# Kernel tuning notes

Measured on AMD Instinct MI355X. Metric: run time of the kernel, lower is better.

## Reference

```python
import jax, jax.numpy as jnp
import numpy as np


def setup_inputs() -> dict:
    key = jax.random.key(0)
    ks = jax.random.split(key, 7)
    B, T, C, H = 8, 2048, 2048, 128
    x = jax.random.normal(ks[0], (B, T, C), dtype=jnp.float32)
    Wq = jax.random.normal(ks[1], (C, H), dtype=jnp.float32) * (C ** -0.5)
    bq = jax.random.normal(ks[2], (H,), dtype=jnp.float32) * 0.02
    Wk = jax.random.normal(ks[3], (C, H), dtype=jnp.float32) * (C ** -0.5)
    bk = jax.random.normal(ks[4], (H,), dtype=jnp.float32) * 0.02
    Wv = jax.random.normal(ks[5], (C, H), dtype=jnp.float32) * (C ** -0.5)
    bv = jax.random.normal(ks[6], (H,), dtype=jnp.float32) * 0.02
    return {"x": x, "Wq": Wq, "bq": bq, "Wk": Wk, "bk": bk, "Wv": Wv, "bv": bv}


def reference(x, Wq, bq, Wk, bk, Wv, bv):
    # Single-head causal self-attention (dropout in eval mode = identity).
    B, T, C = x.shape
    H = Wq.shape[1]
    Q = jnp.einsum("btc,ch->bth", x, Wq) + bq  # [B,T,H]
    K = jnp.einsum("btc,ch->bth", x, Wk) + bk
    V = jnp.einsum("btc,ch->bth", x, Wv) + bv
    scale = H ** -0.5
    wei = jnp.einsum("bth,bsh->bts", Q, K) * scale  # [B,T,T]
    causal = jnp.tril(jnp.ones((T, T), dtype=bool))
    wei = jnp.where(causal, wei, -jnp.inf)
    wei = jax.nn.softmax(wei, axis=-1)
    out = jnp.einsum("bts,bsh->bth", wei, V)  # [B,T,H]
    return out
```

## Files before the change

kernel.cpp:

```cpp
#include <hip/hip_runtime.h>

typedef float f32x4 __attribute__((ext_vector_type(4)));
typedef short short8 __attribute__((ext_vector_type(8)));
typedef unsigned short ushort8 __attribute__((ext_vector_type(8)));

#define WS_Q  786432
#define WS_K  2883584
#define WS_VT 4980736

__device__ __forceinline__ unsigned short f2bf(float x) {
    unsigned u = __float_as_uint(x);
    u += 0x7FFFu + ((u >> 16) & 1u);
    return (unsigned short)(u >> 16);
}

__device__ __forceinline__ int swz128(int row, int cbyte) {
    return row * 128 + (cbyte ^ ((row & 7) << 4));
}

__global__ __launch_bounds__(256) void wt_kernel(const float* __restrict__ Wq,
        const float* __restrict__ Wk, const float* __restrict__ Wv,
        unsigned short* __restrict__ ws) {
    __shared__ __align__(16) unsigned short tile[64][136];
    int mat = blockIdx.x >> 5, ct = blockIdx.x & 31;
    const float* W = (mat == 0) ? Wq : ((mat == 1) ? Wk : Wv);
    int cbase = ct * 64;
    int tid = threadIdx.x;
#pragma unroll
    for (int p = 0; p < 8; p++) {
        int fidx = p * 256 + tid;
        int row = fidx >> 5;
        int c4 = (fidx & 31) << 2;
        float4 v = *(const float4*)&W[(size_t)(cbase + row) * 128 + c4];
        tile[row][c4 + 0] = f2bf(v.x);
        tile[row][c4 + 1] = f2bf(v.y);
        tile[row][c4 + 2] = f2bf(v.z);
        tile[row][c4 + 3] = f2bf(v.w);
    }
    __syncthreads();
    int h = tid >> 1, seg = tid & 1;
    unsigned short* dst = ws + mat * 262144 + (ct * 2 + seg) * 4096 + h * 32;
#pragma unroll
    for (int q4 = 0; q4 < 4; q4++) {
        ushort8 pk;
#pragma unroll
        for (int e = 0; e < 8; e++) pk[e] = tile[seg * 32 + q4 * 8 + e][h];
        *(ushort8*)(dst + q4 * 8) = pk;
    }
}

__global__ __launch_bounds__(256, 3) void qkv_kernel(const float* __restrict__ x,
        const float* __restrict__ bq, const float* __restrict__ bk,
        const float* __restrict__ bv, unsigned short* __restrict__ ws) {
    __shared__ __align__(16) unsigned short lds[4][6144];
    int bid = blockIdx.x;
    int g = bid / 24, j = bid - g * 24;
    int which = j >> 3;
    int mt = g * 8 + (j & 7);
    const unsigned short* WTt = ws + which * 262144;
    const float* x0 = x + (size_t)mt * 64 * 2048;
    int tid = threadIdx.x, lane = tid & 63, wid = tid >> 6;
    int lr = lane & 15, lg = lane >> 4;
    int m0 = (wid >> 1) * 32, n0 = (wid & 1) * 64;

    const float* bias = (which == 0) ? bq : ((which == 1) ? bk : bv);
    float bb[4];
#pragma unroll
    for (int j2 = 0; j2 < 4; j2++) bb[j2] = bias[n0 + j2 * 16 + lr];
    asm volatile("" : "+v"(bb[0]), "+v"(bb[1]), "+v"(bb[2]), "+v"(bb[3]));
    asm volatile("s_waitcnt vmcnt(0)" ::: "memory");

    int rowA = tid >> 2, ca = tid & 3;
    const float* aSrc = x0 + (size_t)rowA * 2048 + ca * 8;
    int aDst = rowA * 64 + ((ca ^ ((rowA >> 1) & 3)) << 4);

    int bsrc0, bsrc1, bdst0, bdst1;
    {
        int idx0 = (0 * 4 + wid) * 64 + lane;
        int h0 = idx0 >> 2, c0 = idx0 & 3;
        bsrc0 = h0 * 32 + ((c0 ^ ((h0 >> 1) & 3)) << 3);
        bdst0 = (0 * 4 + wid) * 1024;
        int idx1 = (1 * 4 + wid) * 64 + lane;
        int h1 = idx1 >> 2, c1 = idx1 & 3;
        bsrc1 = h1 * 32 + ((c1 ^ ((h1 >> 1) & 3)) << 3);
        bdst1 = (1 * 4 + wid) * 1024;
    }

    int aOff0, aOff1, bOff0, bOff1, bOff2, bOff3;
    {
        int r0 = m0 + 0 * 16 + lr; aOff0 = r0 * 64 + ((lg ^ ((r0 >> 1) & 3)) << 4);
        int r1 = m0 + 1 * 16 + lr; aOff1 = r1 * 64 + ((lg ^ ((r1 >> 1) & 3)) << 4);
        int s0 = n0 + 0 * 16 + lr; bOff0 = s0 * 64 + ((lg ^ ((s0 >> 1) & 3)) << 4);
        int s1 = n0 + 1 * 16 + lr; bOff1 = s1 * 64 + ((lg ^ ((s1 >> 1) & 3)) << 4);
        int s2 = n0 + 2 * 16 + lr; bOff2 = s2 * 64 + ((lg ^ ((s2 >> 1) & 3)) << 4);
        int s3 = n0 + 3 * 16 + lr; bOff3 = s3 * 64 + ((lg ^ ((s3 >> 1) & 3)) << 4);
    }

    f32x4 acc[2][4];
#pragma unroll
    for (int i = 0; i < 2; i++)
#pragma unroll
        for (int j3 = 0; j3 < 4; j3++) acc[i][j3] = (f32x4){0.f, 0.f, 0.f, 0.f};
    float4 rA[4][2];

#define ISSUE_A(SLOT, T) do { \
        const float* ap_ = aSrc + (size_t)(T) * 32; \
        rA[SLOT][0] = *(const float4*)ap_; \
        rA[SLOT][1] = *(const float4*)(ap_ + 4); \
    } while (0)
#define ISSUE_B(BUF, T) do { \
        const unsigned short* bs_ = WTt + (size_t)(T) * 4096; \
        char* bd_ = (char*)&lds[BUF][2048]; \
        __builtin_amdgcn_global_load_lds((const __attribute__((address_space(1))) unsigned*)(bs_ + bsrc0), \
            (__attribute__((address_space(3))) unsigned*)(bd_ + bdst0), 16, 0, 0); \
        __builtin_amdgcn_global_load_lds((const __attribute__((address_space(1))) unsigned*)(bs_ + bsrc1), \
            (__attribute__((address_space(3))) unsigned*)(bd_ + bdst1), 16, 0, 0); \
    } while (0)
#define WRITE_A(SLOT, BUF) do { \
        const float* f_ = (const float*)&rA[SLOT][0]; \
        ushort8 pk_; \
        pk_[0] = f2bf(f_[0]); pk_[1] = f2bf(f_[1]); pk_[2] = f2bf(f_[2]); pk_[3] = f2bf(f_[3]); \
        pk_[4] = f2bf(f_[4]); pk_[5] = f2bf(f_[5]); pk_[6] = f2bf(f_[6]); pk_[7] = f2bf(f_[7]); \
        *(ushort8*)((char*)&lds[BUF][0] + aDst) = pk_; \
    } while (0)

#define QKV_BODY(U, T, STAGE, WAIT4, WAIT0, WRITE, BAR) do { \
        const char* Ab_ = (const char*)&lds[U][0]; \
        const char* Bb_ = (const char*)&lds[U][2048]; \
        short8 av0 = *(const short8*)(Ab_ + aOff0); \
        short8 av1 = *(const short8*)(Ab_ + aOff1); \
        short8 bv0 = *(const short8*)(Bb_ + bOff0); \
        short8 bv1 = *(const short8*)(Bb_ + bOff1); \
        short8 bv2 = *(const short8*)(Bb_ + bOff2); \
        short8 bv3 = *(const short8*)(Bb_ + bOff3); \
        if (STAGE) { ISSUE_A(((T) + 3) & 3, (T) + 3); ISSUE_B(((U) + 3) & 3, (T) + 3); } \
        acc[0][0] = __builtin_amdgcn_mfma_f32_16x16x32_bf16(av0, bv0, acc[0][0], 0, 0, 0); \
        acc[0][1] = __builtin_amdgcn_mfma_f32_16x16x32_bf16(av0, bv1, acc[0][1], 0, 0, 0); \
        acc[0][2] = __builtin_amdgcn_mfma_f32_16x16x32_bf16(av0, bv2, acc[0][2], 0, 0, 0); \
        acc[0][3] = __builtin_amdgcn_mfma_f32_16x16x32_bf16(av0, bv3, acc[0][3], 0, 0, 0); \
        acc[1][0] = __builtin_amdgcn_mfma_f32_16x16x32_bf16(av1, bv0, acc[1][0], 0, 0, 0); \
        acc[1][1] = __builtin_amdgcn_mfma_f32_16x16x32_bf16(av1, bv1, acc[1][1], 0, 0, 0); \
        acc[1][2] = __builtin_amdgcn_mfma_f32_16x16x32_bf16(av1, bv2, acc[1][2], 0, 0, 0); \
        acc[1][3] = __builtin_amdgcn_mfma_f32_16x16x32_bf16(av1, bv3, acc[1][3], 0, 0, 0); \
        if (STAGE)      { asm volatile("s_waitcnt vmcnt(8)" ::: "memory"); } \
        else if (WAIT4) { asm volatile("s_waitcnt vmcnt(4)" ::: "memory"); } \
        else if (WAIT0) { asm volatile("s_waitcnt vmcnt(0)" ::: "memory"); } \
        if (WRITE) { \
            WRITE_A(((T) + 1) & 3, ((U) + 1) & 3); \
            asm volatile("s_waitcnt lgkmcnt(0)" ::: "memory"); \
        } \
        if (BAR) __builtin_amdgcn_s_barrier(); \
    } while (0)

    ISSUE_A(0, 0); ISSUE_B(0, 0);
    ISSUE_A(1, 1); ISSUE_B(1, 1);
    ISSUE_A(2, 2); ISSUE_B(2, 2);
    asm volatile("s_waitcnt vmcnt(8)" ::: "memory");
    WRITE_A(0, 0);
    asm volatile("s_waitcnt lgkmcnt(0)" ::: "memory");
    __builtin_amdgcn_s_barrier();

    for (int to = 0; to < 15; to++) {
        int T0 = to * 4;
        QKV_BODY(0, T0 + 0, true, false, false, true, true);
        QKV_BODY(1, T0 + 1, true, false, false, true, true);
        QKV_BODY(2, T0 + 2, true, false, false, true, true);
        QKV_BODY(3, T0 + 3, true, false, false, true, true);
    }
    QKV_BODY(0, 60, true,  false, false, true,  true);
    QKV_BODY(1, 61, false, true,  false, true,  true);
    QKV_BODY(2, 62, false, false, true,  true,  true);
    QKV_BODY(3, 63, false, false, false, false, false);

    if (which < 2) {
        unsigned short* outp = ws + ((which == 0) ? WS_Q : WS_K);
        float sc = (which == 0) ? 0.08838834764831845f : 1.0f;
#pragma unroll
        for (int i = 0; i < 2; i++)
#pragma unroll
            for (int j3 = 0; j3 < 4; j3++) {
                int h = n0 + j3 * 16 + lr;
#pragma unroll
                for (int r = 0; r < 4; r++) {
                    int t = mt * 64 + m0 + i * 16 + (lg << 2) + r;
                    outp[(size_t)t * 128 + h] = f2bf((acc[i][j3][r] + bb[j3]) * sc);
                }
            }
    } else {
        __syncthreads();
        unsigned short* sm = &lds[0][0];
#pragma unroll
        for (int i = 0; i < 2; i++)
#pragma unroll
            for (int j3 = 0; j3 < 4; j3++) {
                int h = n0 + j3 * 16 + lr;
#pragma unroll
                for (int r = 0; r < 4; r++) {
                    int tl = m0 + i * 16 + (lg << 2) + r;
                    sm[tl * 136 + h] = f2bf(acc[i][j3][r] + bb[j3]);
                }
            }
        __syncthreads();
        int h = tid & 127, seg = tid >> 7;
        int b2 = mt >> 5;
        int tin = (mt & 31) * 64 + seg * 32;
        unsigned short* vt = ws + WS_VT + ((size_t)b2 * 128 + h) * 2048 + tin;
#pragma unroll
        for (int q4 = 0; q4 < 4; q4++) {
            ushort8 pk;
#pragma unroll
            for (int e = 0; e < 8; e++) pk[e] = sm[(seg * 32 + q4 * 8 + e) * 136 + h];
            *(ushort8*)(vt + q4 * 8) = pk;
        }
    }
#undef QKV_BODY
#undef WRITE_A
#undef ISSUE_B
#undef ISSUE_A
}

__global__ __launch_bounds__(256, 2) void attn_kernel(const unsigned short* __restrict__ ws,
        float* __restrict__ out) {
    __shared__ __align__(16) float o_lds[4][32][128];
    __shared__ float ml[4][2][32];
    int b = blockIdx.x;
    int qi = 63 - (int)blockIdx.y;
    int qbase = qi * 32;
    int tid = threadIdx.x, lane = tid & 63, w = tid >> 6;
    int lr = lane & 15, lg = lane >> 4;
    const unsigned short* Qb = ws + WS_Q + (size_t)b * 2048 * 128;
    const unsigned short* Kb = ws + WS_K + (size_t)b * 2048 * 128;
    const unsigned short* Vt = ws + WS_VT + (size_t)b * 128 * 2048;
    char* p_lds = (char*)&o_lds[w][0][0];

    short8 qf[2][4];
#pragma unroll
    for (int i = 0; i < 2; i++)
#pragma unroll
        for (int kf = 0; kf < 4; kf++)
            qf[i][kf] = *(const short8*)&Qb[(size_t)(qbase + i * 16 + lr) * 128 + kf * 32 + lg * 8];

    f32x4 o[2][8];
#pragma unroll
    for (int i = 0; i < 2; i++)
#pragma unroll
        for (int jn = 0; jn < 8; jn++) o[i][jn] = (f32x4){0.f, 0.f, 0.f, 0.f};
    float mrow[2][4], lrow[2][4];
#pragma unroll
    for (int i = 0; i < 2; i++)
#pragma unroll
        for (int r = 0; r < 4; r++) { mrow[i][r] = -__builtin_inff(); lrow[i][r] = 0.f; }

    int ntiles = qi / 2 + 1;
    for (int ti = w; ti < ntiles; ti += 4) {
        int sb = ti * 64;
        f32x4 s[2][4];
#pragma unroll
        for (int i = 0; i < 2; i++)
#pragma unroll
            for (int nf = 0; nf < 4; nf++) s[i][nf] = (f32x4){0.f, 0.f, 0.f, 0.f};
        {
            short8 kb[4][4];
#pragma unroll
            for (int nf = 0; nf < 4; nf++)
#pragma unroll
                for (int kf = 0; kf < 4; kf++)
                    kb[nf][kf] = *(const short8*)&Kb[(size_t)(sb + nf * 16 + lr) * 128 + kf * 32 + lg * 8];
#pragma unroll
            for (int kf = 0; kf < 4; kf++)
#pragma unroll
                for (int i = 0; i < 2; i++)
#pragma unroll
                    for (int nf = 0; nf < 4; nf++)
                        s[i][nf] = __builtin_amdgcn_mfma_f32_16x16x32_bf16(qf[i][kf], kb[nf][kf], s[i][nf], 0, 0, 0);
        }
        if (sb + 63 > qbase) {
#pragma unroll
            for (int i = 0; i < 2; i++)
#pragma unroll
                for (int nf = 0; nf < 4; nf++)
#pragma unroll
                    for (int r = 0; r < 4; r++) {
                        int sg = sb + nf * 16 + lr;
                        int qg = qbase + i * 16 + (lg << 2) + r;
                        if (sg > qg) s[i][nf][r] = -__builtin_inff();
                    }
        }
        float alpha[2][4];
#pragma unroll
        for (int i = 0; i < 2; i++)
#pragma unroll
            for (int r = 0; r < 4; r++) {
                float pm = fmaxf(fmaxf(s[i][0][r], s[i][1][r]), fmaxf(s[i][2][r], s[i][3][r]));
                pm = fmaxf(pm, __shfl_xor(pm, 1));
                pm = fmaxf(pm, __shfl_xor(pm, 2));
                pm = fmaxf(pm, __shfl_xor(pm, 4));
                pm = fmaxf(pm, __shfl_xor(pm, 8));
                float mn = fmaxf(mrow[i][r], pm);
                alpha[i][r] = __expf(mrow[i][r] - mn);
                mrow[i][r] = mn;
            }
#pragma unroll
        for (int i = 0; i < 2; i++)
#pragma unroll
            for (int r = 0; r < 4; r++) {
                float rs = 0.f;
#pragma unroll
                for (int nf = 0; nf < 4; nf++) {
                    float p = __expf(s[i][nf][r] - mrow[i][r]);
                    s[i][nf][r] = p;
                    rs += p;
                }
                rs += __shfl_xor(rs, 1);
                rs += __shfl_xor(rs, 2);
                rs += __shfl_xor(rs, 4);
                rs += __shfl_xor(rs, 8);
                lrow[i][r] = lrow[i][r] * alpha[i][r] + rs;
            }
#pragma unroll
        for (int i = 0; i < 2; i++)
#pragma unroll
            for (int jn = 0; jn < 8; jn++)
#pragma unroll
                for (int r = 0; r < 4; r++) o[i][jn][r] *= alpha[i][r];
#pragma unroll
        for (int i = 0; i < 2; i++)
#pragma unroll
            for (int nf = 0; nf < 4; nf++)
#pragma unroll
                for (int r = 0; r < 4; r++) {
                    int row = i * 16 + (lg << 2) + r;
                    int cb2 = (nf * 16 + lr) * 2;
                    *(unsigned short*)(p_lds + swz128(row, cb2)) = f2bf(s[i][nf][r]);
                }
        asm volatile("s_waitcnt lgkmcnt(0)" ::: "memory");
        short8 pa[2][2];
#pragma unroll
        for (int i = 0; i < 2; i++)
#pragma unroll
            for (int kf = 0; kf < 2; kf++)
                pa[i][kf] = *(const short8*)(p_lds + swz128(i * 16 + lr, kf * 64 + lg * 16));
        short8 vb[8][2];
#pragma unroll
        for (int nf = 0; nf < 8; nf++)
#pragma unroll
            for (int kf = 0; kf < 2; kf++)
                vb[nf][kf] = *(const short8*)&Vt[(size_t)(nf * 16 + lr) * 2048 + sb + kf * 32 + lg * 8];
#pragma unroll
        for (int i = 0; i < 2; i++)
#pragma unroll
            for (int nf = 0; nf < 8; nf++)
#pragma unroll
                for (int kf = 0; kf < 2; kf++)
                    o[i][nf] = __builtin_amdgcn_mfma_f32_16x16x32_bf16(pa[i][kf], vb[nf][kf], o[i][nf], 0, 0, 0);
    }
#pragma unroll
    for (int i = 0; i < 2; i++)
#pragma unroll
        for (int r = 0; r < 4; r++) {
            int q = i * 16 + (lg << 2) + r;
            ml[w][0][q] = mrow[i][r];
            ml[w][1][q] = lrow[i][r];
        }
    asm volatile("s_waitcnt lgkmcnt(0)" ::: "memory");
#pragma unroll
    for (int i = 0; i < 2; i++)
#pragma unroll
        for (int jn = 0; jn < 8; jn++)
#pragma unroll
            for (int r = 0; r < 4; r++)
                o_lds[w][i * 16 + (lg << 2) + r][jn * 16 + lr] = o[i][jn][r];
    __syncthreads();
    int q = tid >> 3, h0 = (tid & 7) << 4;
    float mg = fmaxf(fmaxf(ml[0][0][q], ml[1][0][q]), fmaxf(ml[2][0][q], ml[3][0][q]));
    float scw[4], den = 0.f;
#pragma unroll
    for (int w4 = 0; w4 < 4; w4++) {
        scw[w4] = __expf(ml[w4][0][q] - mg);
        den += scw[w4] * ml[w4][1][q];
    }
    float inv = 1.0f / den;
    float* op = out + ((size_t)b * 2048 + qbase + q) * 128 + h0;
#pragma unroll
    for (int jj = 0; jj < 4; jj++) {
        f32x4 a4 = (f32x4){0.f, 0.f, 0.f, 0.f};
#pragma unroll
        for (int w4 = 0; w4 < 4; w4++) {
            f32x4 v = *(const f32x4*)&o_lds[w4][q][h0 + jj * 4];
            a4 += scw[w4] * v;
        }
        a4 *= inv;
        *(f32x4*)(op + jj * 4) = a4;
    }
}

extern "C" void kernel_launch(void* const* d_in, const int* in_sizes, int n_in,
                              void* d_out, int out_size, void* d_ws, size_t ws_size,
                              hipStream_t stream) {
    (void)in_sizes; (void)n_in; (void)out_size; (void)ws_size;
    const float* x  = (const float*)d_in[0];
    const float* Wq = (const float*)d_in[1];
    const float* bq = (const float*)d_in[2];
    const float* Wk = (const float*)d_in[3];
    const float* bk = (const float*)d_in[4];
    const float* Wv = (const float*)d_in[5];
    const float* bv = (const float*)d_in[6];
    unsigned short* ws = (unsigned short*)d_ws;
    float* out = (float*)d_out;

    wt_kernel<<<96, 256, 0, stream>>>(Wq, Wk, Wv, ws);
    qkv_kernel<<<768, 256, 0, stream>>>(x, bq, bk, bv, ws);
    attn_kernel<<<dim3(8, 64), 256, 0, stream>>>(ws, out);
}
```

Baseline: 106.9 us.

## Enlarge QKV projection tile to 128 rows with triple-buffered LDS pipeline

Result: slower. 246.5 us (+130.6%).

```diff
diff --git a/kernel.cpp b/kernel.cpp
--- a/kernel.cpp
+++ b/kernel.cpp
@@ -12,6 +12,15 @@
     unsigned u = __float_as_uint(x);
     u += 0x7FFFu + ((u >> 16) & 1u);
     return (unsigned short)(u >> 16);
+}
+
+__device__ __forceinline__ short8 cvt8(float4 lo, float4 hi) {
+    union { unsigned u[4]; short8 s; } r;
+    asm("v_cvt_pk_bf16_f32 %0, %1, %2" : "=v"(r.u[0]) : "v"(lo.x), "v"(lo.y));
+    asm("v_cvt_pk_bf16_f32 %0, %1, %2" : "=v"(r.u[1]) : "v"(lo.z), "v"(lo.w));
+    asm("v_cvt_pk_bf16_f32 %0, %1, %2" : "=v"(r.u[2]) : "v"(hi.x), "v"(hi.y));
+    asm("v_cvt_pk_bf16_f32 %0, %1, %2" : "=v"(r.u[3]) : "v"(hi.z), "v"(hi.w));
+    return r.s;
 }
 
 __device__ __forceinline__ int swz128(int row, int cbyte) {
@@ -52,88 +61,90 @@
 __global__ __launch_bounds__(256, 3) void qkv_kernel(const float* __restrict__ x,
         const float* __restrict__ bq, const float* __restrict__ bk,
         const float* __restrict__ bv, unsigned short* __restrict__ ws) {
-    __shared__ __align__(16) unsigned short lds[4][6144];
+    __shared__ __align__(16) char lds_raw[3][16384];
     int bid = blockIdx.x;
-    int g = bid / 24, j = bid - g * 24;
-    int which = j >> 3;
-    int mt = g * 8 + (j & 7);
-    const unsigned short* WTt = ws + which * 262144;
-    const float* x0 = x + (size_t)mt * 64 * 2048;
+    int matrix = bid >> 7;
+    int strip = bid & 127;
+    const unsigned short* WTt = ws + matrix * 262144;
+    const float* x0 = x + (size_t)strip * 128 * 2048;
     int tid = threadIdx.x, lane = tid & 63, wid = tid >> 6;
     int lr = lane & 15, lg = lane >> 4;
-    int m0 = (wid >> 1) * 32, n0 = (wid & 1) * 64;
-
-    const float* bias = (which == 0) ? bq : ((which == 1) ? bk : bv);
+    int m0 = (wid >> 1) * 64, n0 = (wid & 1) * 64;
+
+    const float* bias = (matrix == 0) ? bq : ((matrix == 1) ? bk : bv);
     float bb[4];
 #pragma unroll
     for (int j2 = 0; j2 < 4; j2++) bb[j2] = bias[n0 + j2 * 16 + lr];
     asm volatile("" : "+v"(bb[0]), "+v"(bb[1]), "+v"(bb[2]), "+v"(bb[3]));
     asm volatile("s_waitcnt vmcnt(0)" ::: "memory");
 
-    int rowA = tid >> 2, ca = tid & 3;
-    const float* aSrc = x0 + (size_t)rowA * 2048 + ca * 8;
-    int aDst = rowA * 64 + ((ca ^ ((rowA >> 1) & 3)) << 4);
+    int rowA = tid >> 1, hf = tid & 1;
+    const float* aSrc = x0 + (size_t)rowA * 2048 + hf * 16;
+    int aDst0 = rowA * 64 + (((hf * 2 + 0) ^ ((rowA >> 1) & 3)) << 4);
+    int aDst1 = rowA * 64 + (((hf * 2 + 1) ^ ((rowA >> 1) & 3)) << 4);
 
     int bsrc0, bsrc1, bdst0, bdst1;
     {
-        int idx0 = (0 * 4 + wid) * 64 + lane;
-        int h0 = idx0 >> 2, c0 = idx0 & 3;
-        bsrc0 = h0 * 32 + ((c0 ^ ((h0 >> 1) & 3)) << 3);
-        bdst0 = (0 * 4 + wid) * 1024;
-        int idx1 = (1 * 4 + wid) * 64 + lane;
-        int h1 = idx1 >> 2, c1 = idx1 & 3;
-        bsrc1 = h1 * 32 + ((c1 ^ ((h1 >> 1) & 3)) << 3);
-        bdst1 = (1 * 4 + wid) * 1024;
-    }
-
-    int aOff0, aOff1, bOff0, bOff1, bOff2, bOff3;
+        int sig0 = wid * 64 + lane;
+        int r0 = sig0 >> 2, s0 = (sig0 & 3) ^ ((r0 >> 1) & 3);
+        bsrc0 = r0 * 32 + s0 * 8;  bdst0 = wid * 1024;
+        int sig1 = (4 + wid) * 64 + lane;
+        int r1 = sig1 >> 2, s1 = (sig1 & 3) ^ ((r1 >> 1) & 3);
+        bsrc1 = r1 * 32 + s1 * 8;  bdst1 = (4 + wid) * 1024;
+    }
+
+    int aOff0, aOff1, aOff2, aOff3, bOff0, bOff1, bOff2, bOff3;
     {
         int r0 = m0 + 0 * 16 + lr; aOff0 = r0 * 64 + ((lg ^ ((r0 >> 1) & 3)) << 4);
         int r1 = m0 + 1 * 16 + lr; aOff1 = r1 * 64 + ((lg ^ ((r1 >> 1) & 3)) << 4);
-        int s0 = n0 + 0 * 16 + lr; bOff0 = s0 * 64 + ((lg ^ ((s0 >> 1) & 3)) << 4);
-        int s1 = n0 + 1 * 16 + lr; bOff1 = s1 * 64 + ((lg ^ ((s1 >> 1) & 3)) << 4);
-        int s2 = n0 + 2 * 16 + lr; bOff2 = s2 * 64 + ((lg ^ ((s2 >> 1) & 3)) << 4);
-        int s3 = n0 + 3 * 16 + lr; bOff3 = s3 * 64 + ((lg ^ ((s3 >> 1) & 3)) << 4);
-    }
-
-    f32x4 acc[2][4];
-#pragma unroll
-    for (int i = 0; i < 2; i++)
+        int r2 = m0 + 2 * 16 + lr; aOff2 = r2 * 64 + ((lg ^ ((r2 >> 1) & 3)) << 4);
+        int r3 = m0 + 3 * 16 + lr; aOff3 = r3 * 64 + ((lg ^ ((r3 >> 1) & 3)) << 4);
+        int h0 = n0 + 0 * 16 + lr; bOff0 = 8192 + h0 * 64 + ((lg ^ ((h0 >> 1) & 3)) << 4);
+        int h1 = n0 + 1 * 16 + lr; bOff1 = 8192 + h1 * 64 + ((lg ^ ((h1 >> 1) & 3)) << 4);
+        int h2 = n0 + 2 * 16 + lr; bOff2 = 8192 + h2 * 64 + ((lg ^ ((h2 >> 1) & 3)) << 4);
+        int h3 = n0 + 3 * 16 + lr; bOff3 = 8192 + h3 * 64 + ((lg ^ ((h3 >> 1) & 3)) << 4);
+    }
+
+    f32x4 acc[4][4];
+#pragma unroll
+    for (int i = 0; i < 4; i++)
 #pragma unroll
         for (int j3 = 0; j3 < 4; j3++) acc[i][j3] = (f32x4){0.f, 0.f, 0.f, 0.f};
-    float4 rA[4][2];
+    float4 rA[2][4];
 
 #define ISSUE_A(SLOT, T) do { \
         const float* ap_ = aSrc + (size_t)(T) * 32; \
         rA[SLOT][0] = *(const float4*)ap_; \
         rA[SLOT][1] = *(const float4*)(ap_ + 4); \
+        rA[SLOT][2] = *(const float4*)(ap_ + 8); \
+        rA[SLOT][3] = *(const float4*)(ap_ + 12); \
     } while (0)
 #define ISSUE_B(BUF, T) do { \
         const unsigned short* bs_ = WTt + (size_t)(T) * 4096; \
-        char* bd_ = (char*)&lds[BUF][2048]; \
+        char* bd_ = &lds_raw[BUF][8192]; \
         __builtin_amdgcn_global_load_lds((const __attribute__((address_space(1))) unsigned*)(bs_ + bsrc0), \
             (__attribute__((address_space(3))) unsigned*)(bd_ + bdst0), 16, 0, 0); \
         __builtin_amdgcn_global_load_lds((const __attribute__((address_space(1))) unsigned*)(bs_ + bsrc1), \
             (__attribute__((address_space(3))) unsigned*)(bd_ + bdst1), 16, 0, 0); \
     } while (0)
 #define WRITE_A(SLOT, BUF) do { \
-        const float* f_ = (const float*)&rA[SLOT][0]; \
-        ushort8 pk_; \
-        pk_[0] = f2bf(f_[0]); pk_[1] = f2bf(f_[1]); pk_[2] = f2bf(f_[2]); pk_[3] = f2bf(f_[3]); \
-        pk_[4] = f2bf(f_[4]); pk_[5] = f2bf(f_[5]); pk_[6] = f2bf(f_[6]); pk_[7] = f2bf(f_[7]); \
-        *(ushort8*)((char*)&lds[BUF][0] + aDst) = pk_; \
+        short8 p0_ = cvt8(rA[SLOT][0], rA[SLOT][1]); \
+        short8 p1_ = cvt8(rA[SLOT][2], rA[SLOT][3]); \
+        *(short8*)(&lds_raw[BUF][0] + aDst0) = p0_; \
+        *(short8*)(&lds_raw[BUF][0] + aDst1) = p1_; \
     } while (0)
 
-#define QKV_BODY(U, T, STAGE, WAIT4, WAIT0, WRITE, BAR) do { \
-        const char* Ab_ = (const char*)&lds[U][0]; \
-        const char* Bb_ = (const char*)&lds[U][2048]; \
-        short8 av0 = *(const short8*)(Ab_ + aOff0); \
-        short8 av1 = *(const short8*)(Ab_ + aOff1); \
-        short8 bv0 = *(const short8*)(Bb_ + bOff0); \
-        short8 bv1 = *(const short8*)(Bb_ + bOff1); \
-        short8 bv2 = *(const short8*)(Bb_ + bOff2); \
-        short8 bv3 = *(const short8*)(Bb_ + bOff3); \
-        if (STAGE) { ISSUE_A(((T) + 3) & 3, (T) + 3); ISSUE_B(((U) + 3) & 3, (T) + 3); } \
+#define QKV_BODY(U, T, STAGE, WAIT0, WRITE, BAR) do { \
+        const char* Lb_ = &lds_raw[U][0]; \
+        short8 av0 = *(const short8*)(Lb_ + aOff0); \
+        short8 av1 = *(const short8*)(Lb_ + aOff1); \
+        short8 av2 = *(const short8*)(Lb_ + aOff2); \
+        short8 av3 = *(const short8*)(Lb_ + aOff3); \
+        short8 bv0 = *(const short8*)(Lb_ + bOff0); \
+        short8 bv1 = *(const short8*)(Lb_ + bOff1); \
+        short8 bv2 = *(const short8*)(Lb_ + bOff2); \
+        short8 bv3 = *(const short8*)(Lb_ + bOff3); \
+        if (STAGE) { ISSUE_A((T) & 1, (T) + 2); ISSUE_B(((U) + 2) % 3, (T) + 2); } \
         acc[0][0] = __builtin_amdgcn_mfma_f32_16x16x32_bf16(av0, bv0, acc[0][0], 0, 0, 0); \
         acc[0][1] = __builtin_amdgcn_mfma_f32_16x16x32_bf16(av0, bv1, acc[0][1], 0, 0, 0); \
         acc[0][2] = __builtin_amdgcn_mfma_f32_16x16x32_bf16(av0, bv2, acc[0][2], 0, 0, 0); \
@@ -142,11 +153,18 @@
         acc[1][1] = __builtin_amdgcn_mfma_f32_16x16x32_bf16(av1, bv1, acc[1][1], 0, 0, 0); \
         acc[1][2] = __builtin_amdgcn_mfma_f32_16x16x32_bf16(av1, bv2, acc[1][2], 0, 0, 0); \
         acc[1][3] = __builtin_amdgcn_mfma_f32_16x16x32_bf16(av1, bv3, acc[1][3], 0, 0, 0); \
-        if (STAGE)      { asm volatile("s_waitcnt vmcnt(8)" ::: "memory"); } \
-        else if (WAIT4) { asm volatile("s_waitcnt vmcnt(4)" ::: "memory"); } \
+        acc[2][0] = __builtin_amdgcn_mfma_f32_16x16x32_bf16(av2, bv0, acc[2][0], 0, 0, 0); \
+        acc[2][1] = __builtin_amdgcn_mfma_f32_16x16x32_bf16(av2, bv1, acc[2][1], 0, 0, 0); \
+        acc[2][2] = __builtin_amdgcn_mfma_f32_16x16x32_bf16(av2, bv2, acc[2][2], 0, 0, 0); \
+        acc[2][3] = __builtin_amdgcn_mfma_f32_16x16x32_bf16(av2, bv3, acc[2][3], 0, 0, 0); \
+        acc[3][0] = __builtin_amdgcn_mfma_f32_16x16x32_bf16(av3, bv0, acc[3][0], 0, 0, 0); \
+        acc[3][1] = __builtin_amdgcn_mfma_f32_16x16x32_bf16(av3, bv1, acc[3][1], 0, 0, 0); \
+        acc[3][2] = __builtin_amdgcn_mfma_f32_16x16x32_bf16(av3, bv2, acc[3][2], 0, 0, 0); \
+        acc[3][3] = __builtin_amdgcn_mfma_f32_16x16x32_bf16(av3, bv3, acc[3][3], 0, 0, 0); \
+        if (STAGE)      { asm volatile("s_waitcnt vmcnt(6)" ::: "memory"); } \
         else if (WAIT0) { asm volatile("s_waitcnt vmcnt(0)" ::: "memory"); } \
         if (WRITE) { \
-            WRITE_A(((T) + 1) & 3, ((U) + 1) & 3); \
+            WRITE_A(((T) + 1) & 1, ((U) + 1) % 3); \
             asm volatile("s_waitcnt lgkmcnt(0)" ::: "memory"); \
         } \
         if (BAR) __builtin_amdgcn_s_barrier(); \
@@ -154,43 +172,41 @@
 
     ISSUE_A(0, 0); ISSUE_B(0, 0);
     ISSUE_A(1, 1); ISSUE_B(1, 1);
-    ISSUE_A(2, 2); ISSUE_B(2, 2);
-    asm volatile("s_waitcnt vmcnt(8)" ::: "memory");
+    asm volatile("s_waitcnt vmcnt(6)" ::: "memory");
     WRITE_A(0, 0);
     asm volatile("s_waitcnt lgkmcnt(0)" ::: "memory");
     __builtin_amdgcn_s_barrier();
 
-    for (int to = 0; to < 15; to++) {
-        int T0 = to * 4;
-        QKV_BODY(0, T0 + 0, true, false, false, true, true);
-        QKV_BODY(1, T0 + 1, true, false, false, true, true);
-        QKV_BODY(2, T0 + 2, true, false, false, true, true);
-        QKV_BODY(3, T0 + 3, true, false, false, true, true);
-    }
-    QKV_BODY(0, 60, true,  false, false, true,  true);
-    QKV_BODY(1, 61, false, true,  false, true,  true);
-    QKV_BODY(2, 62, false, false, true,  true,  true);
-    QKV_BODY(3, 63, false, false, false, false, false);
-
-    if (which < 2) {
-        unsigned short* outp = ws + ((which == 0) ? WS_Q : WS_K);
-        float sc = (which == 0) ? 0.08838834764831845f : 1.0f;
-#pragma unroll
-        for (int i = 0; i < 2; i++)
+    for (int to = 0; to < 20; to++) {
+        int T0 = to * 3;
+        QKV_BODY(0, T0 + 0, true, false, true, true);
+        QKV_BODY(1, T0 + 1, true, false, true, true);
+        QKV_BODY(2, T0 + 2, true, false, true, true);
+    }
+    QKV_BODY(0, 60, true,  false, true,  true);
+    QKV_BODY(1, 61, true,  false, true,  true);
+    QKV_BODY(2, 62, false, true,  true,  true);
+    QKV_BODY(0, 63, false, false, false, false);
+
+    if (matrix < 2) {
+        unsigned short* outp = ws + ((matrix == 0) ? WS_Q : WS_K);
+        float sc = (matrix == 0) ? 0.08838834764831845f : 1.0f;
+#pragma unroll
+        for (int i = 0; i < 4; i++)
 #pragma unroll
             for (int j3 = 0; j3 < 4; j3++) {
                 int h = n0 + j3 * 16 + lr;
 #pragma unroll
                 for (int r = 0; r < 4; r++) {
-                    int t = mt * 64 + m0 + i * 16 + (lg << 2) + r;
-                    outp[(size_t)t * 128 + h] = f2bf((acc[i][j3][r] + bb[j3]) * sc);
+                    size_t t = (size_t)strip * 128 + m0 + i * 16 + (lg << 2) + r;
+                    outp[t * 128 + h] = f2bf((acc[i][j3][r] + bb[j3]) * sc);
                 }
             }
     } else {
         __syncthreads();
-        unsigned short* sm = &lds[0][0];
-#pragma unroll
-        for (int i = 0; i < 2; i++)
+        unsigned short* sm = (unsigned short*)&lds_raw[0][0];
+#pragma unroll
+        for (int i = 0; i < 4; i++)
 #pragma unroll
             for (int j3 = 0; j3 < 4; j3++) {
                 int h = n0 + j3 * 16 + lr;
@@ -201,16 +217,16 @@
                 }
             }
         __syncthreads();
-        int h = tid & 127, seg = tid >> 7;
-        int b2 = mt >> 5;
-        int tin = (mt & 31) * 64 + seg * 32;
-        unsigned short* vt = ws + WS_VT + ((size_t)b2 * 128 + h) * 2048 + tin;
-#pragma unroll
-        for (int q4 = 0; q4 < 4; q4++) {
+        int h2 = tid >> 1, seg = tid & 1;
+        int batch = strip >> 4;
+        int tin = (strip & 15) * 128 + seg * 64;
+        unsigned short* vt = ws + WS_VT + ((size_t)batch * 128 + h2) * 2048 + tin;
+#pragma unroll
+        for (int q8 = 0; q8 < 8; q8++) {
             ushort8 pk;
 #pragma unroll
-            for (int e = 0; e < 8; e++) pk[e] = sm[(seg * 32 + q4 * 8 + e) * 136 + h];
-            *(ushort8*)(vt + q4 * 8) = pk;
+            for (int e = 0; e < 8; e++) pk[e] = sm[(seg * 64 + q8 * 8 + e) * 136 + h2];
+            *(ushort8*)(vt + q8 * 8) = pk;
         }
     }
 #undef QKV_BODY
@@ -409,6 +425,6 @@
     float* out = (float*)d_out;
 
     wt_kernel<<<96, 256, 0, stream>>>(Wq, Wk, Wv, ws);
-    qkv_kernel<<<768, 256, 0, stream>>>(x, bq, bk, bv, ws);
+    qkv_kernel<<<384, 256, 0, stream>>>(x, bq, bk, bv, ws);
     attn_kernel<<<dim3(8, 64), 256, 0, stream>>>(ws, out);
 }
```

## Restructure QKV projection to 64-wide K tiles with double buffering

Applied to the files above, without the earlier changes.

Measured after the change: 113.2 us. 1.06x slower.

```diff
diff --git a/kernel.cpp b/kernel.cpp
--- a/kernel.cpp
+++ b/kernel.cpp
@@ -3,6 +3,9 @@
 typedef float f32x4 __attribute__((ext_vector_type(4)));
 typedef short short8 __attribute__((ext_vector_type(8)));
 typedef unsigned short ushort8 __attribute__((ext_vector_type(8)));
+
+#define AS1 __attribute__((address_space(1)))
+#define AS3 __attribute__((address_space(3)))
 
 #define WS_Q  786432
 #define WS_K  2883584
@@ -12,6 +15,15 @@
     unsigned u = __float_as_uint(x);
     u += 0x7FFFu + ((u >> 16) & 1u);
     return (unsigned short)(u >> 16);
+}
+
+__device__ __forceinline__ short8 cvt8(float4 lo, float4 hi) {
+    union { unsigned u[4]; short8 s; } r;
+    asm("v_cvt_pk_bf16_f32 %0, %1, %2" : "=v"(r.u[0]) : "v"(lo.x), "v"(lo.y));
+    asm("v_cvt_pk_bf16_f32 %0, %1, %2" : "=v"(r.u[1]) : "v"(lo.z), "v"(lo.w));
+    asm("v_cvt_pk_bf16_f32 %0, %1, %2" : "=v"(r.u[2]) : "v"(hi.x), "v"(hi.y));
+    asm("v_cvt_pk_bf16_f32 %0, %1, %2" : "=v"(r.u[3]) : "v"(hi.z), "v"(hi.w));
+    return r.s;
 }
 
 __device__ __forceinline__ int swz128(int row, int cbyte) {
@@ -39,61 +51,53 @@
     }
     __syncthreads();
     int h = tid >> 1, seg = tid & 1;
-    unsigned short* dst = ws + mat * 262144 + (ct * 2 + seg) * 4096 + h * 32;
+    unsigned short* base = ws + mat * 262144 + ct * 8192 + h * 64;
 #pragma unroll
     for (int q4 = 0; q4 < 4; q4++) {
         ushort8 pk;
 #pragma unroll
         for (int e = 0; e < 8; e++) pk[e] = tile[seg * 32 + q4 * 8 + e][h];
-        *(ushort8*)(dst + q4 * 8) = pk;
+        int g = seg * 4 + q4;
+        *(ushort8*)(base + ((g ^ (h & 7)) << 3)) = pk;
     }
 }
 
 __global__ __launch_bounds__(256, 3) void qkv_kernel(const float* __restrict__ x,
         const float* __restrict__ bq, const float* __restrict__ bk,
         const float* __restrict__ bv, unsigned short* __restrict__ ws) {
-    __shared__ __align__(16) unsigned short lds[4][6144];
+    __shared__ __align__(16) char lds[2][24576];
     int bid = blockIdx.x;
     int g = bid / 24, j = bid - g * 24;
-    int which = j >> 3;
+    int matrix = j >> 3;
     int mt = g * 8 + (j & 7);
-    const unsigned short* WTt = ws + which * 262144;
+    const unsigned short* WTt = ws + matrix * 262144;
     const float* x0 = x + (size_t)mt * 64 * 2048;
     int tid = threadIdx.x, lane = tid & 63, wid = tid >> 6;
     int lr = lane & 15, lg = lane >> 4;
     int m0 = (wid >> 1) * 32, n0 = (wid & 1) * 64;
 
-    const float* bias = (which == 0) ? bq : ((which == 1) ? bk : bv);
-    float bb[4];
-#pragma unroll
-    for (int j2 = 0; j2 < 4; j2++) bb[j2] = bias[n0 + j2 * 16 + lr];
-    asm volatile("" : "+v"(bb[0]), "+v"(bb[1]), "+v"(bb[2]), "+v"(bb[3]));
-    asm volatile("s_waitcnt vmcnt(0)" ::: "memory");
-
-    int rowA = tid >> 2, ca = tid & 3;
-    const float* aSrc = x0 + (size_t)rowA * 2048 + ca * 8;
-    int aDst = rowA * 64 + ((ca ^ ((rowA >> 1) & 3)) << 4);
-
-    int bsrc0, bsrc1, bdst0, bdst1;
+    int rowA = tid >> 2, qa = tid & 3;
+    const float* aSrc = x0 + (size_t)rowA * 2048 + qa * 16;
+    int aD0 = rowA * 128 + ((((qa * 2 + 0)) ^ (rowA & 7)) << 4);
+    int aD1 = rowA * 128 + ((((qa * 2 + 1)) ^ (rowA & 7)) << 4);
+
+    int aOff00, aOff01, aOff10, aOff11;
+    int bOff00, bOff01, bOff10, bOff11, bOff20, bOff21, bOff30, bOff31;
     {
-        int idx0 = (0 * 4 + wid) * 64 + lane;
-        int h0 = idx0 >> 2, c0 = idx0 & 3;
-        bsrc0 = h0 * 32 + ((c0 ^ ((h0 >> 1) & 3)) << 3);
-        bdst0 = (0 * 4 + wid) * 1024;
-        int idx1 = (1 * 4 + wid) * 64 + lane;
-        int h1 = idx1 >> 2, c1 = idx1 & 3;
-        bsrc1 = h1 * 32 + ((c1 ^ ((h1 >> 1) & 3)) << 3);
-        bdst1 = (1 * 4 + wid) * 1024;
-    }
-
-    int aOff0, aOff1, bOff0, bOff1, bOff2, bOff3;
-    {
-        int r0 = m0 + 0 * 16 + lr; aOff0 = r0 * 64 + ((lg ^ ((r0 >> 1) & 3)) << 4);
-        int r1 = m0 + 1 * 16 + lr; aOff1 = r1 * 64 + ((lg ^ ((r1 >> 1) & 3)) << 4);
-        int s0 = n0 + 0 * 16 + lr; bOff0 = s0 * 64 + ((lg ^ ((s0 >> 1) & 3)) << 4);
-        int s1 = n0 + 1 * 16 + lr; bOff1 = s1 * 64 + ((lg ^ ((s1 >> 1) & 3)) << 4);
-        int s2 = n0 + 2 * 16 + lr; bOff2 = s2 * 64 + ((lg ^ ((s2 >> 1) & 3)) << 4);
-        int s3 = n0 + 3 * 16 + lr; bOff3 = s3 * 64 + ((lg ^ ((s3 >> 1) & 3)) << 4);
+        int r0 = m0 + lr, r1 = m0 + 16 + lr;
+        aOff00 = r0 * 128 + (((0 * 4 + lg) ^ (r0 & 7)) << 4);
+        aOff01 = r0 * 128 + (((1 * 4 + lg) ^ (r0 & 7)) << 4);
+        aOff10 = r1 * 128 + (((0 * 4 + lg) ^ (r1 & 7)) << 4);
+        aOff11 = r1 * 128 + (((1 * 4 + lg) ^ (r1 & 7)) << 4);
+        int h0 = n0 + lr, h1 = n0 + 16 + lr, h2 = n0 + 32 + lr, h3 = n0 + 48 + lr;
+        bOff00 = 8192 + h0 * 128 + (((0 * 4 + lg) ^ (h0 & 7)) << 4);
+        bOff01 = 8192 + h0 * 128 + (((1 * 4 + lg) ^ (h0 & 7)) << 4);
+        bOff10 = 8192 + h1 * 128 + (((0 * 4 + lg) ^ (h1 & 7)) << 4);
+        bOff11 = 8192 + h1 * 128 + (((1 * 4 + lg) ^ (h1 & 7)) << 4);
+        bOff20 = 8192 + h2 * 128 + (((0 * 4 + lg) ^ (h2 & 7)) << 4);
+        bOff21 = 8192 + h2 * 128 + (((1 * 4 + lg) ^ (h2 & 7)) << 4);
+        bOff30 = 8192 + h3 * 128 + (((0 * 4 + lg) ^ (h3 & 7)) << 4);
+        bOff31 = 8192 + h3 * 128 + (((1 * 4 + lg) ^ (h3 & 7)) << 4);
     }
 
     f32x4 acc[2][4];
@@ -101,80 +105,92 @@
     for (int i = 0; i < 2; i++)
 #pragma unroll
         for (int j3 = 0; j3 < 4; j3++) acc[i][j3] = (f32x4){0.f, 0.f, 0.f, 0.f};
-    float4 rA[4][2];
-
-#define ISSUE_A(SLOT, T) do { \
-        const float* ap_ = aSrc + (size_t)(T) * 32; \
-        rA[SLOT][0] = *(const float4*)ap_; \
-        rA[SLOT][1] = *(const float4*)(ap_ + 4); \
+    float4 rA0, rA1, rA2, rA3;
+
+#define ISSUE_AB(BUF, T) do { \
+        const float* ap_ = aSrc + (size_t)(T) * 64; \
+        rA0 = *(const float4*)ap_;        rA1 = *(const float4*)(ap_ + 4); \
+        rA2 = *(const float4*)(ap_ + 8);  rA3 = *(const float4*)(ap_ + 12); \
+        const unsigned short* bs_ = WTt + (size_t)(T) * 8192 + tid * 8; \
+        char* bd_ = &lds[BUF][8192] + tid * 16; \
+        __builtin_amdgcn_global_load_lds((const AS1 unsigned*)(bs_), \
+            (AS3 unsigned*)(bd_), 16, 0, 0); \
+        __builtin_amdgcn_global_load_lds((const AS1 unsigned*)(bs_ + 2048), \
+            (AS3 unsigned*)(bd_ + 4096), 16, 0, 0); \
+        __builtin_amdgcn_global_load_lds((const AS1 unsigned*)(bs_ + 4096), \
+            (AS3 unsigned*)(bd_ + 8192), 16, 0, 0); \
+        __builtin_amdgcn_global_load_lds((const AS1 unsigned*)(bs_ + 6144), \
+            (AS3 unsigned*)(bd_ + 12288), 16, 0, 0); \
     } while (0)
-#define ISSUE_B(BUF, T) do { \
-        const unsigned short* bs_ = WTt + (size_t)(T) * 4096; \
-        char* bd_ = (char*)&lds[BUF][2048]; \
-        __builtin_amdgcn_global_load_lds((const __attribute__((address_space(1))) unsigned*)(bs_ + bsrc0), \
-            (__attribute__((address_space(3))) unsigned*)(bd_ + bdst0), 16, 0, 0); \
-        __builtin_amdgcn_global_load_lds((const __attribute__((address_space(1))) unsigned*)(bs_ + bsrc1), \
-            (__attribute__((address_space(3))) unsigned*)(bd_ + bdst1), 16, 0, 0); \
+#define WRITE_A(BUF) do { \
+        short8 p0_ = cvt8(rA0, rA1); \
+        short8 p1_ = cvt8(rA2, rA3); \
+        *(short8*)(&lds[BUF][0] + aD0) = p0_; \
+        *(short8*)(&lds[BUF][0] + aD1) = p1_; \
     } while (0)
-#define WRITE_A(SLOT, BUF) do { \
-        const float* f_ = (const float*)&rA[SLOT][0]; \
-        ushort8 pk_; \
-        pk_[0] = f2bf(f_[0]); pk_[1] = f2bf(f_[1]); pk_[2] = f2bf(f_[2]); pk_[3] = f2bf(f_[3]); \
-        pk_[4] = f2bf(f_[4]); pk_[5] = f2bf(f_[5]); pk_[6] = f2bf(f_[6]); pk_[7] = f2bf(f_[7]); \
-        *(ushort8*)((char*)&lds[BUF][0] + aDst) = pk_; \
-    } while (0)
-
-#define QKV_BODY(U, T, STAGE, WAIT4, WAIT0, WRITE, BAR) do { \
-        const char* Ab_ = (const char*)&lds[U][0]; \
-        const char* Bb_ = (const char*)&lds[U][2048]; \
-        short8 av0 = *(const short8*)(Ab_ + aOff0); \
-        short8 av1 = *(const short8*)(Ab_ + aOff1); \
-        short8 bv0 = *(const short8*)(Bb_ + bOff0); \
-        short8 bv1 = *(const short8*)(Bb_ + bOff1); \
-        short8 bv2 = *(const short8*)(Bb_ + bOff2); \
-        short8 bv3 = *(const short8*)(Bb_ + bOff3); \
-        if (STAGE) { ISSUE_A(((T) + 3) & 3, (T) + 3); ISSUE_B(((U) + 3) & 3, (T) + 3); } \
-        acc[0][0] = __builtin_amdgcn_mfma_f32_16x16x32_bf16(av0, bv0, acc[0][0], 0, 0, 0); \
-        acc[0][1] = __builtin_amdgcn_mfma_f32_16x16x32_bf16(av0, bv1, acc[0][1], 0, 0, 0); \
-        acc[0][2] = __builtin_amdgcn_mfma_f32_16x16x32_bf16(av0, bv2, acc[0][2], 0, 0, 0); \
-        acc[0][3] = __builtin_amdgcn_mfma_f32_16x16x32_bf16(av0, bv3, acc[0][3], 0, 0, 0); \
-        acc[1][0] = __builtin_amdgcn_mfma_f32_16x16x32_bf16(av1, bv0, acc[1][0], 0, 0, 0); \
-        acc[1][1] = __builtin_amdgcn_mfma_f32_16x16x32_bf16(av1, bv1, acc[1][1], 0, 0, 0); \
-        acc[1][2] = __builtin_amdgcn_mfma_f32_16x16x32_bf16(av1, bv2, acc[1][2], 0, 0, 0); \
-        acc[1][3] = __builtin_amdgcn_mfma_f32_16x16x32_bf16(av1, bv3, acc[1][3], 0, 0, 0); \
-        if (STAGE)      { asm volatile("s_waitcnt vmcnt(8)" ::: "memory"); } \
-        else if (WAIT4) { asm volatile("s_waitcnt vmcnt(4)" ::: "memory"); } \
-        else if (WAIT0) { asm volatile("s_waitcnt vmcnt(0)" ::: "memory"); } \
-        if (WRITE) { \
-            WRITE_A(((T) + 1) & 3, ((U) + 1) & 3); \
+
+#define QKV_BODY(T, CUR, STAGE, BAR) do { \
+        if (STAGE) ISSUE_AB((CUR) ^ 1, (T) + 1); \
+        const char* Lb_ = &lds[CUR][0]; \
+        short8 a00 = *(const short8*)(Lb_ + aOff00); \
+        short8 a01 = *(const short8*)(Lb_ + aOff01); \
+        short8 a10 = *(const short8*)(Lb_ + aOff10); \
+        short8 a11 = *(const short8*)(Lb_ + aOff11); \
+        short8 b00 = *(const short8*)(Lb_ + bOff00); \
+        short8 b01 = *(const short8*)(Lb_ + bOff01); \
+        short8 b10 = *(const short8*)(Lb_ + bOff10); \
+        short8 b11 = *(const short8*)(Lb_ + bOff11); \
+        short8 b20 = *(const short8*)(Lb_ + bOff20); \
+        short8 b21 = *(const short8*)(Lb_ + bOff21); \
+        short8 b30 = *(const short8*)(Lb_ + bOff30); \
+        short8 b31 = *(const short8*)(Lb_ + bOff31); \
+        __builtin_amdgcn_s_setprio(1); \
+        acc[0][0] = __builtin_amdgcn_mfma_f32_16x16x32_bf16(a00, b00, acc[0][0], 0, 0, 0); \
+        acc[0][1] = __builtin_amdgcn_mfma_f32_16x16x32_bf16(a00, b10, acc[0][1], 0, 0, 0); \
+        acc[0][2] = __builtin_amdgcn_mfma_f32_16x16x32_bf16(a00, b20, acc[0][2], 0, 0, 0); \
+        acc[0][3] = __builtin_amdgcn_mfma_f32_16x16x32_bf16(a00, b30, acc[0][3], 0, 0, 0); \
+        acc[1][0] = __builtin_amdgcn_mfma_f32_16x16x32_bf16(a10, b00, acc[1][0], 0, 0, 0); \
+        acc[1][1] = __builtin_amdgcn_mfma_f32_16x16x32_bf16(a10, b10, acc[1][1], 0, 0, 0); \
+        acc[1][2] = __builtin_amdgcn_mfma_f32_16x16x32_bf16(a10, b20, acc[1][2], 0, 0, 0); \
+        acc[1][3] = __builtin_amdgcn_mfma_f32_16x16x32_bf16(a10, b30, acc[1][3], 0, 0, 0); \
+        acc[0][0] = __builtin_amdgcn_mfma_f32_16x16x32_bf16(a01, b01, acc[0][0], 0, 0, 0); \
+        acc[0][1] = __builtin_amdgcn_mfma_f32_16x16x32_bf16(a01, b11, acc[0][1], 0, 0, 0); \
+        acc[0][2] = __builtin_amdgcn_mfma_f32_16x16x32_bf16(a01, b21, acc[0][2], 0, 0, 0); \
+        acc[0][3] = __builtin_amdgcn_mfma_f32_16x16x32_bf16(a01, b31, acc[0][3], 0, 0, 0); \
+        acc[1][0] = __builtin_amdgcn_mfma_f32_16x16x32_bf16(a11, b01, acc[1][0], 0, 0, 0); \
+        acc[1][1] = __builtin_amdgcn_mfma_f32_16x16x32_bf16(a11, b11, acc[1][1], 0, 0, 0); \
+        acc[1][2] = __builtin_amdgcn_mfma_f32_16x16x32_bf16(a11, b21, acc[1][2], 0, 0, 0); \
+        acc[1][3] = __builtin_amdgcn_mfma_f32_16x16x32_bf16(a11, b31, acc[1][3], 0, 0, 0); \
+        __builtin_amdgcn_s_setprio(0); \
+        if (STAGE) { \
+            asm volatile("s_waitcnt vmcnt(0)" ::: "memory"); \
+            WRITE_A((CUR) ^ 1); \
             asm volatile("s_waitcnt lgkmcnt(0)" ::: "memory"); \
         } \
         if (BAR) __builtin_amdgcn_s_barrier(); \
     } while (0)
 
-    ISSUE_A(0, 0); ISSUE_B(0, 0);
-    ISSUE_A(1, 1); ISSUE_B(1, 1);
-    ISSUE_A(2, 2); ISSUE_B(2, 2);
-    asm volatile("s_waitcnt vmcnt(8)" ::: "memory");
-    WRITE_A(0, 0);
+    ISSUE_AB(0, 0);
+    asm volatile("s_waitcnt vmcnt(0)" ::: "memory");
+    WRITE_A(0);
     asm volatile("s_waitcnt lgkmcnt(0)" ::: "memory");
     __builtin_amdgcn_s_barrier();
 
-    for (int to = 0; to < 15; to++) {
-        int T0 = to * 4;
-        QKV_BODY(0, T0 + 0, true, false, false, true, true);
-        QKV_BODY(1, T0 + 1, true, false, false, true, true);
-        QKV_BODY(2, T0 + 2, true, false, false, true, true);
-        QKV_BODY(3, T0 + 3, true, false, false, true, true);
-    }
-    QKV_BODY(0, 60, true,  false, false, true,  true);
-    QKV_BODY(1, 61, false, true,  false, true,  true);
-    QKV_BODY(2, 62, false, false, true,  true,  true);
-    QKV_BODY(3, 63, false, false, false, false, false);
-
-    if (which < 2) {
-        unsigned short* outp = ws + ((which == 0) ? WS_Q : WS_K);
-        float sc = (which == 0) ? 0.08838834764831845f : 1.0f;
+    for (int t2 = 0; t2 < 15; t2++) {
+        int t = t2 * 2;
+        QKV_BODY(t + 0, 0, true, true);
+        QKV_BODY(t + 1, 1, true, true);
+    }
+    QKV_BODY(30, 0, true,  true);
+    QKV_BODY(31, 1, false, false);
+
+    const float* bias = (matrix == 0) ? bq : ((matrix == 1) ? bk : bv);
+    float bb[4];
+#pragma unroll
+    for (int j3 = 0; j3 < 4; j3++) bb[j3] = bias[n0 + j3 * 16 + lr];
+    if (matrix < 2) {
+        unsigned short* outp = ws + ((matrix == 0) ? WS_Q : WS_K);
+        float sc = (matrix == 0) ? 0.08838834764831845f : 1.0f;
 #pragma unroll
         for (int i = 0; i < 2; i++)
 #pragma unroll
@@ -182,13 +198,13 @@
                 int h = n0 + j3 * 16 + lr;
 #pragma unroll
                 for (int r = 0; r < 4; r++) {
-                    int t = mt * 64 + m0 + i * 16 + (lg << 2) + r;
-                    outp[(size_t)t * 128 + h] = f2bf((acc[i][j3][r] + bb[j3]) * sc);
+                    size_t t = (size_t)mt * 64 + m0 + i * 16 + (lg << 2) + r;
+                    outp[t * 128 + h] = f2bf((acc[i][j3][r] + bb[j3]) * sc);
                 }
             }
     } else {
         __syncthreads();
-        unsigned short* sm = &lds[0][0];
+        unsigned short* sm = (unsigned short*)&lds[0][0];
 #pragma unroll
         for (int i = 0; i < 2; i++)
 #pragma unroll
@@ -215,8 +231,7 @@
     }
 #undef QKV_BODY
 #undef WRITE_A
-#undef ISSUE_B
-#undef ISSUE_A
+#undef ISSUE_AB
 }
 
 __global__ __launch_bounds__(256, 2) void attn_kernel(const unsigned short* __restrict__ ws,
```
